# Optimization experiments

Measured on AMD Instinct MI355X. Metric: run time of the kernel, lower is better.

The kernel has to match this reference:

```python
import jax, jax.numpy as jnp
import numpy as np

N_NODES = 100000
N_EDGES = 1600000
OBS_DIMS = 128
HID = 128
ACT_DIMS = 8
NUM_GRAPHS = 256
NEG_SLOPE = 0.2


def setup_inputs() -> dict:
    key = jax.random.key(0)
    ks = jax.random.split(key, 20)
    inp = {}
    inp["x"] = jax.random.normal(ks[0], (N_NODES, OBS_DIMS), dtype=jnp.float32)
    inp["edge_index"] = jax.random.randint(ks[1], (2, N_EDGES), 0, N_NODES, dtype=jnp.int64)
    inp["batch"] = jnp.sort(jax.random.randint(ks[2], (N_NODES,), 0, NUM_GRAPHS, dtype=jnp.int64))
    # GATConv layer params (heads=1): W [out,in], att_src/att_dst [out], bias [out]
    dims = [(HID, OBS_DIMS), (HID, HID), (HID, HID)]
    for i, (o, c) in enumerate(dims, start=1):
        k = 3 + 4 * (i - 1)
        inp[f"W{i}"] = jax.random.normal(ks[k], (o, c), dtype=jnp.float32) * (1.0 / np.sqrt(c))
        inp[f"as{i}"] = jax.random.normal(ks[k + 1], (o,), dtype=jnp.float32) * 0.1
        inp[f"ad{i}"] = jax.random.normal(ks[k + 2], (o,), dtype=jnp.float32) * 0.1
        inp[f"b{i}"] = jnp.zeros((o,), dtype=jnp.float32)
    inp["Wl"] = jax.random.normal(ks[15], (ACT_DIMS, HID), dtype=jnp.float32) * (1.0 / np.sqrt(HID))
    inp["bl"] = jnp.zeros((ACT_DIMS,), dtype=jnp.float32)
    return inp


def _gat_conv(x, src, dst, W, att_src, att_dst, bias):
    """PyG GATConv with heads=1, negative_slope=0.2 (self-loops already in src/dst)."""
    h = x @ W.T                                  # [N, out]
    a_s = h @ att_src                            # [N]
    a_d = h @ att_dst                            # [N]
    e = jax.nn.leaky_relu(a_s[src] + a_d[dst], NEG_SLOPE)   # [E] per-edge logits
    m = jax.ops.segment_max(e, dst, num_segments=N_NODES)   # segment softmax (stable)
    ex = jnp.exp(e - m[dst])
    denom = jax.ops.segment_sum(ex, dst, num_segments=N_NODES)
    alpha = ex / denom[dst]                      # [E]
    out = jax.ops.segment_sum(alpha[:, None] * h[src], dst, num_segments=N_NODES)
    return out + bias


def reference(x, edge_index, batch, W1, as1, ad1, b1, W2, as2, ad2, b2,
              W3, as3, ad3, b3, Wl, bl):
    # add self-loops (PyG GATConv default add_self_loops=True)
    loop = jnp.arange(N_NODES, dtype=edge_index.dtype)
    src = jnp.concatenate([edge_index[0], loop])
    dst = jnp.concatenate([edge_index[1], loop])

    h = jax.nn.relu(_gat_conv(x, src, dst, W1, as1, ad1, b1))
    h = jax.nn.relu(_gat_conv(h, src, dst, W2, as2, ad2, b2))
    h = jax.nn.relu(_gat_conv(h, src, dst, W3, as3, ad3, b3))
    h = jnp.tanh(h @ Wl.T + bl)                  # [N, act_dims]

    # global_mean_pool over graph ids
    sums = jax.ops.segment_sum(h, batch, num_segments=NUM_GRAPHS)
    cnts = jax.ops.segment_sum(jnp.ones((h.shape[0],), h.dtype), batch, num_segments=NUM_GRAPHS)
    return sums / jnp.clip(cnts, 1.0)[:, None]
```

## Files before the change

kernel.cpp:

```cpp
#include <hip/hip_runtime.h>

#define N_NODES 100000
#define N_EDGES 1600000
#define E_TOT   1700000
#define HID     128
#define NGRAPH  256
#define NBUCK   196
#define NBLK1   831
#define HSTRIDE 832

typedef unsigned short ushort_t;
typedef unsigned int uint_t;
typedef __attribute__((ext_vector_type(8))) short bf16x8;
typedef __attribute__((ext_vector_type(4))) float f32x4;

__device__ inline ushort_t f2bf(float f) {
  uint_t u = __float_as_uint(f);
  return (ushort_t)((u + 0x7FFFu + ((u >> 16) & 1u)) >> 16);
}

__global__ __launch_bounds__(256) void k_wcvt(const float* __restrict__ W0,
                                              const float* __restrict__ W1,
                                              const float* __restrict__ W2,
                                              const float* __restrict__ Wlh,
                                              ushort_t* __restrict__ Wb,
                                              ushort_t* __restrict__ Wlb) {
  int i = blockIdx.x * 256 + threadIdx.x;
  if (i < 49152) {
    const float* src = (i < 16384) ? W0 : (i < 32768 ? W1 : W2);
    Wb[i] = f2bf(src[i & 16383]);
  } else if (i < 51200) {
    int j = i - 49152;
    Wlb[j] = (j < 1024) ? f2bf(Wlh[j]) : (ushort_t)0;
  }
}

__global__ __launch_bounds__(256) void k_b1(const int* __restrict__ ei,
                                            int* __restrict__ hist) {
  __shared__ int h[NBUCK];
  const int t = threadIdx.x;
  for (int i = t; i < NBUCK; i += 256) h[i] = 0;
  __syncthreads();
  const int e0 = blockIdx.x * 2048;
#pragma unroll
  for (int u = 0; u < 8; ++u) {
    int e = e0 + u * 256 + t;
    if (e < E_TOT) {
      int dst = (e < N_EDGES) ? ei[N_EDGES + e] : (e - N_EDGES);
      atomicAdd(&h[dst >> 9], 1);
    }
  }
  __syncthreads();
  for (int i = t; i < NBUCK; i += 256) hist[i * HSTRIDE + blockIdx.x] = h[i];
}

__global__ __launch_bounds__(1024) void k_bscan1(int* __restrict__ hist,
                                                 int* __restrict__ btot) {
  __shared__ int sh[1024];
  const int b = blockIdx.x, t = threadIdx.x;
  int v = (t < NBLK1) ? hist[b * HSTRIDE + t] : 0;
  sh[t] = v;
  __syncthreads();
  for (int off = 1; off < 1024; off <<= 1) {
    int x = (t >= off) ? sh[t - off] : 0;
    __syncthreads();
    sh[t] += x;
    __syncthreads();
  }
  if (t < NBLK1) hist[b * HSTRIDE + t] = sh[t] - v;
  if (t == 1023) btot[b] = sh[1023];
}

__global__ void k_bscan2(const int* __restrict__ btot, int* __restrict__ bbase) {
  if (threadIdx.x == 0 && blockIdx.x == 0) {
    int run = 0;
    for (int i = 0; i < NBUCK; ++i) { bbase[i] = run; run += btot[i]; }
    bbase[NBUCK] = run;
  }
}

__global__ __launch_bounds__(256) void k_b2(const int* __restrict__ ei,
                                            const int* __restrict__ hist,
                                            const int* __restrict__ bbase,
                                            int2* __restrict__ buf) {
  __shared__ int h[NBUCK];
  __shared__ int base2[NBUCK];
  const int t = threadIdx.x;
  for (int i = t; i < NBUCK; i += 256) {
    h[i] = 0;
    base2[i] = bbase[i] + hist[i * HSTRIDE + blockIdx.x];
  }
  __syncthreads();
  const int e0 = blockIdx.x * 2048;
#pragma unroll
  for (int u = 0; u < 8; ++u) {
    int e = e0 + u * 256 + t;
    if (e < E_TOT) {
      int src, dst;
      if (e < N_EDGES) { src = ei[e]; dst = ei[N_EDGES + e]; }
      else             { src = e - N_EDGES; dst = src; }
      int bk = dst >> 9;
      int r = atomicAdd(&h[bk], 1);
      buf[base2[bk] + r] = int2{src, dst};
    }
  }
}

__global__ __launch_bounds__(512) void k_b3(const int2* __restrict__ buf,
                                            const int* __restrict__ bbase,
                                            int* __restrict__ indptr,
                                            int* __restrict__ csr_src) {
  __shared__ int cnt[512];
  __shared__ int cur[512];
  const int b = blockIdx.x, t = threadIdx.x;
  cnt[t] = 0;
  __syncthreads();
  const int es = bbase[b], ee = bbase[b + 1];
  for (int e = es + t; e < ee; e += 512) {
    int2 p = buf[e];
    atomicAdd(&cnt[p.y & 511], 1);
  }
  __syncthreads();
  int v = cnt[t];
  cur[t] = v;
  __syncthreads();
  for (int off = 1; off < 512; off <<= 1) {
    int x = (t >= off) ? cur[t - off] : 0;
    __syncthreads();
    cur[t] += x;
    __syncthreads();
  }
  int excl = cur[t] - v;
  int n = b * 512 + t;
  if (n < N_NODES) indptr[n] = es + excl;
  if (b == NBUCK - 1 && t == 0) indptr[N_NODES] = E_TOT;
  __syncthreads();
  cur[t] = es + excl;
  __syncthreads();
  for (int e = es + t; e < ee; e += 512) {
    int2 p = buf[e];
    int pos = atomicAdd(&cur[p.y & 511], 1);
    csr_src[pos] = p.x;
  }
}

template <bool IN_F32>
__global__ __launch_bounds__(256) void k_gemm(const void* __restrict__ Xin,
                                              const ushort_t* __restrict__ Wbl,
                                              const float* __restrict__ att_s,
                                              const float* __restrict__ att_d,
                                              ushort_t* __restrict__ Hb,
                                              float* __restrict__ As,
                                              float* __restrict__ Ad) {
  __shared__ ushort_t Wl[128 * 128];
  __shared__ ushort_t Xl[64 * 128];
  const int t = threadIdx.x;
  const int row0 = blockIdx.x * 64;

#pragma unroll
  for (int i = 0; i < 8; ++i) {
    int idx = (t + i * 256) << 3;
    int o = idx >> 7, c = idx & 127;
    uint4 wv = *(const uint4*)&Wbl[idx];
    *(uint4*)((char*)Wl + o * 256 + ((c * 2) ^ ((o & 7) << 4))) = wv;
  }
  if (IN_F32) {
    const float* X = (const float*)Xin;
#pragma unroll
    for (int i = 0; i < 8; ++i) {
      int idx = (t + i * 256) << 2;
      int r = idx >> 7, c = idx & 127;
      int row = row0 + r;
      float4 xv = (row < N_NODES) ? *(const float4*)&X[row * 128 + c]
                                  : float4{0.f, 0.f, 0.f, 0.f};
      ushort4 xb{f2bf(xv.x), f2bf(xv.y), f2bf(xv.z), f2bf(xv.w)};
      *(ushort4*)((char*)Xl + r * 256 + ((c * 2) ^ ((r & 7) << 4))) = xb;
    }
  } else {
    const ushort_t* X = (const ushort_t*)Xin;
#pragma unroll
    for (int i = 0; i < 4; ++i) {
      int idx = (t + i * 256) << 3;
      int r = idx >> 7, c = idx & 127;
      int row = row0 + r;
      uint4 xv = (row < N_NODES) ? *(const uint4*)&X[row * 128 + c]
                                 : uint4{0u, 0u, 0u, 0u};
      *(uint4*)((char*)Xl + r * 256 + ((c * 2) ^ ((r & 7) << 4))) = xv;
    }
  }
  __syncthreads();

  const int wv = t >> 6;
  const int lane = t & 63;
  const int lr = lane & 15;
  const int lg = lane >> 4;
  f32x4 acc[8] = {};

#pragma unroll
  for (int ks = 0; ks < 4; ++ks) {
    const int kbyte = ks * 64 + lg * 16;
    const int arow = wv * 16 + lr;
    bf16x8 afrag = *(const bf16x8*)((char*)Xl + arow * 256 +
                                    (kbyte ^ ((arow & 7) << 4)));
#pragma unroll
    for (int ot = 0; ot < 8; ++ot) {
      const int orow = ot * 16 + lr;
      bf16x8 bfrag = *(const bf16x8*)((char*)Wl + orow * 256 +
                                      (kbyte ^ ((orow & 7) << 4)));
      acc[ot] = __builtin_amdgcn_mfma_f32_16x16x32_bf16(afrag, bfrag, acc[ot],
                                                        0, 0, 0);
    }
  }

  float ps[4] = {0.f, 0.f, 0.f, 0.f}, pd[4] = {0.f, 0.f, 0.f, 0.f};
#pragma unroll
  for (int ot = 0; ot < 8; ++ot) {
    float sa = att_s[ot * 16 + lr], sd = att_d[ot * 16 + lr];
#pragma unroll
    for (int j = 0; j < 4; ++j) {
      ps[j] += acc[ot][j] * sa;
      pd[j] += acc[ot][j] * sd;
    }
  }
#pragma unroll
  for (int m = 1; m < 16; m <<= 1) {
#pragma unroll
    for (int j = 0; j < 4; ++j) {
      ps[j] += __shfl_xor(ps[j], m);
      pd[j] += __shfl_xor(pd[j], m);
    }
  }
  if (lr == 0) {
#pragma unroll
    for (int j = 0; j < 4; ++j) {
      int row = row0 + wv * 16 + lg * 4 + j;
      if (row < N_NODES) { As[row] = ps[j]; Ad[row] = pd[j]; }
    }
  }

  __syncthreads();
#pragma unroll
  for (int ot = 0; ot < 8; ++ot)
#pragma unroll
    for (int j = 0; j < 4; ++j) {
      int r = wv * 16 + lg * 4 + j;
      int cbyte = (ot * 16 + lr) * 2;
      *(ushort_t*)((char*)Xl + r * 256 + (cbyte ^ ((r & 7) << 4))) =
          f2bf(acc[ot][j]);
    }
  __syncthreads();
#pragma unroll
  for (int i = 0; i < 4; ++i) {
    int idx = t + i * 256;
    int r = idx >> 4, u = idx & 15;
    int row = row0 + r;
    if (row < N_NODES)
      *(uint4*)&Hb[row * 128 + u * 8] =
          *(const uint4*)((char*)Xl + r * 256 + ((u * 16) ^ ((r & 7) << 4)));
  }
}

__global__ __launch_bounds__(256) void k_agg(const ushort_t* __restrict__ Hb,
                                             const float* __restrict__ a_s,
                                             const float* __restrict__ a_d,
                                             const int* __restrict__ indptr,
                                             const int* __restrict__ csr_src,
                                             const float* __restrict__ bias,
                                             ushort_t* __restrict__ OUTb) {
  const int lane = threadIdx.x & 63;
  const int wid  = threadIdx.x >> 6;
  const int half = lane >> 5;
  const int l32  = lane & 31;
  const int n = blockIdx.x * 8 + wid * 2 + half;

  const int start = indptr[n];
  const int deg   = indptr[n + 1] - start;
  const float adn = a_d[n];

  int   s0 = csr_src[start + ((l32 < deg) ? l32 : 0)];
  float w0 = 0.f;
  if (l32 < deg) {
    float e = a_s[s0] + adn;
    e = (e > 0.f) ? e : 0.2f * e;
    w0 = __expf(e);
  }
  float wsum = w0;

  const int degA = __shfl(deg, 0);
  const int degB = __shfl(deg, 32);
  const int degM = max(degA, degB);

  const int q  = lane >> 4;
  const int qe = q & 1;
  const int srcbase = (q >> 1) << 5;
  const int ch = (lane & 15) << 3;
  float acc8[8] = {0.f, 0.f, 0.f, 0.f, 0.f, 0.f, 0.f, 0.f};

#define FMA8(W4, A)                                                         \
  {                                                                         \
    float a_ = (A);                                                         \
    acc8[0] += a_ * __uint_as_float((W4).x << 16);                          \
    acc8[1] += a_ * __uint_as_float((W4).x & 0xFFFF0000u);                  \
    acc8[2] += a_ * __uint_as_float((W4).y << 16);                          \
    acc8[3] += a_ * __uint_as_float((W4).y & 0xFFFF0000u);                  \
    acc8[4] += a_ * __uint_as_float((W4).z << 16);                          \
    acc8[5] += a_ * __uint_as_float((W4).z & 0xFFFF0000u);                  \
    acc8[6] += a_ * __uint_as_float((W4).w << 16);                          \
    acc8[7] += a_ * __uint_as_float((W4).w & 0xFFFF0000u);                  \
  }

  {
    const int npM = (min(degM, 32) + 1) >> 1;
    float av[8]; int sv[8];
#pragma unroll
    for (int u = 0; u < 8; ++u) {
      int sl = srcbase + ((u << 1) + qe);
      av[u] = __shfl(w0, sl);
      sv[u] = __shfl(s0, sl);
    }
    uint4 hvA[4], hvB[4];
#pragma unroll
    for (int u = 0; u < 4; ++u)
      if (u < npM) hvA[u] = *(const uint4*)&Hb[sv[u] * 128 + ch];
#pragma unroll
    for (int u = 0; u < 4; ++u)
      if (u + 4 < npM) hvB[u] = *(const uint4*)&Hb[sv[u + 4] * 128 + ch];
#pragma unroll
    for (int u = 0; u < 4; ++u)
      if (u < npM) FMA8(hvA[u], av[u]);
#pragma unroll
    for (int u = 0; u < 4; ++u)
      if (u + 4 < npM) FMA8(hvB[u], av[u + 4]);
    for (int u0 = 8; u0 < npM; ++u0) {
      int sl = srcbase + ((u0 << 1) + qe);
      float a = __shfl(w0, sl);
      int s = __shfl(s0, sl);
      uint4 hv = *(const uint4*)&Hb[s * 128 + ch];
      FMA8(hv, a);
    }
  }
  for (int base = 32; base < degM; base += 32) {
    int j = base + l32;
    int mys = csr_src[start + ((j < deg) ? j : 0)];
    float myw = 0.f;
    if (j < deg) {
      float e = a_s[mys] + adn;
      e = (e > 0.f) ? e : 0.2f * e;
      myw = __expf(e);
    }
    wsum += myw;
    const int npM = (min(degM - base, 32) + 1) >> 1;
    for (int u0 = 0; u0 < npM; ++u0) {
      int sl = srcbase + ((u0 << 1) + qe);
      float a = __shfl(myw, sl);
      int s = __shfl(mys, sl);
      uint4 hv = *(const uint4*)&Hb[s * 128 + ch];
      FMA8(hv, a);
    }
  }
#undef FMA8

#pragma unroll
  for (int m = 1; m < 32; m <<= 1) wsum += __shfl_xor(wsum, m);
  const float inv = 1.0f / wsum;

#pragma unroll
  for (int c = 0; c < 8; ++c)
    acc8[c] = (acc8[c] + __shfl_xor(acc8[c], 16)) * inv;

  if (qe == 0) {
    float4 b0 = *(const float4*)&bias[ch];
    float4 b1 = *(const float4*)&bias[ch + 4];
    ushort4 lo{f2bf(fmaxf(acc8[0] + b0.x, 0.f)),
               f2bf(fmaxf(acc8[1] + b0.y, 0.f)),
               f2bf(fmaxf(acc8[2] + b0.z, 0.f)),
               f2bf(fmaxf(acc8[3] + b0.w, 0.f))};
    ushort4 hi{f2bf(fmaxf(acc8[4] + b1.x, 0.f)),
               f2bf(fmaxf(acc8[5] + b1.y, 0.f)),
               f2bf(fmaxf(acc8[6] + b1.z, 0.f)),
               f2bf(fmaxf(acc8[7] + b1.w, 0.f))};
    *(ushort4*)&OUTb[n * 128 + ch] = lo;
    *(ushort4*)&OUTb[n * 128 + ch + 4] = hi;
  }
}

__global__ __launch_bounds__(256) void k_head(const ushort_t* __restrict__ Hb,
                                              const ushort_t* __restrict__ Wlb,
                                              const float* __restrict__ bl,
                                              float* __restrict__ h8) {
  __shared__ ushort_t Xl[64 * 128];
  __shared__ ushort_t Wls[16 * 128];
  const int t = threadIdx.x;
  const int row0 = blockIdx.x * 64;

  {
    int idx = t * 8;
    int o = idx >> 7, c = idx & 127;
    uint4 wv = *(const uint4*)&Wlb[idx];
    *(uint4*)((char*)Wls + o * 256 + ((c * 2) ^ ((o & 7) << 4))) = wv;
  }
#pragma unroll
  for (int i = 0; i < 4; ++i) {
    int idx = (t + i * 256) << 3;
    int r = idx >> 7, c = idx & 127;
    int row = row0 + r;
    uint4 xv = (row < N_NODES) ? *(const uint4*)&Hb[row * 128 + c]
                               : uint4{0u, 0u, 0u, 0u};
    *(uint4*)((char*)Xl + r * 256 + ((c * 2) ^ ((r & 7) << 4))) = xv;
  }
  __syncthreads();

  const int wv = t >> 6;
  const int lane = t & 63;
  const int lr = lane & 15;
  const int lg = lane >> 4;
  f32x4 acc = {};
#pragma unroll
  for (int ks = 0; ks < 4; ++ks) {
    const int kbyte = ks * 64 + lg * 16;
    const int arow = wv * 16 + lr;
    bf16x8 afrag = *(const bf16x8*)((char*)Xl + arow * 256 +
                                    (kbyte ^ ((arow & 7) << 4)));
    bf16x8 bfrag = *(const bf16x8*)((char*)Wls + lr * 256 +
                                    (kbyte ^ ((lr & 7) << 4)));
    acc = __builtin_amdgcn_mfma_f32_16x16x32_bf16(afrag, bfrag, acc, 0, 0, 0);
  }

  if (lr < 8) {
    float b = bl[lr];
#pragma unroll
    for (int j = 0; j < 4; ++j) {
      int row = row0 + wv * 16 + lg * 4 + j;
      if (row < N_NODES) h8[row * 8 + lr] = tanhf(acc[j] + b);
    }
  }
}

__global__ __launch_bounds__(256) void k_pool(const float* __restrict__ h8,
                                              const int* __restrict__ batch,
                                              float* __restrict__ out) {
  int g = blockIdx.x;
  __shared__ int bounds[2];
  if (threadIdx.x < 2) {
    int target = g + threadIdx.x;
    int lo = 0, hi = N_NODES;
    while (lo < hi) {
      int mid = (lo + hi) >> 1;
      if (batch[mid] < target) lo = mid + 1; else hi = mid;
    }
    bounds[threadIdx.x] = lo;
  }
  __syncthreads();
  int lo = bounds[0], hi = bounds[1];
  int ch = threadIdx.x & 7;
  float acc = 0.f;
  for (int n = lo + (threadIdx.x >> 3); n < hi; n += 32)
    acc += h8[n * 8 + ch];

  __shared__ float red[256];
  red[threadIdx.x] = acc;
  __syncthreads();
  for (int off = 128; off >= 8; off >>= 1) {
    if (threadIdx.x < off) red[threadIdx.x] += red[threadIdx.x + off];
    __syncthreads();
  }
  if (threadIdx.x < 8)
    out[g * 8 + threadIdx.x] = red[threadIdx.x] / fmaxf((float)(hi - lo), 1.0f);
}

extern "C" void kernel_launch(void* const* d_in, const int* in_sizes, int n_in,
                              void* d_out, int out_size, void* d_ws, size_t ws_size,
                              hipStream_t stream) {
  const float* x   = (const float*)d_in[0];
  const int*   ei  = (const int*)d_in[1];
  const int*   bat = (const int*)d_in[2];
  const float* Wm[3]  = {(const float*)d_in[3],  (const float*)d_in[7],  (const float*)d_in[11]};
  const float* asv[3] = {(const float*)d_in[4],  (const float*)d_in[8],  (const float*)d_in[12]};
  const float* adv[3] = {(const float*)d_in[5],  (const float*)d_in[9],  (const float*)d_in[13]};
  const float* bv[3]  = {(const float*)d_in[6],  (const float*)d_in[10], (const float*)d_in[14]};
  const float* Wl  = (const float*)d_in[15];
  const float* bl  = (const float*)d_in[16];
  float* out = (float*)d_out;

  char* w = (char*)d_ws;
  ushort_t* Hb   = (ushort_t*)(w + 0);
  ushort_t* hB2  = (ushort_t*)(w + 25600000);
  float* a_s     = (float*)(w + 51200000);
  float* a_d     = (float*)(w + 51600000);
  int*   indptr  = (int*)  (w + 52000000);
  int*   csr     = (int*)  (w + 52400128);
  int2*  buf1    = (int2*) (w + 59200128);
  int*   hist    = (int*)  (w + 72800128);
  int*   btot    = (int*)  (w + 73452416);
  int*   bbase   = (int*)  (w + 73453200);
  float* h8      = (float*)(w + 73454000);
  ushort_t* Wb   = (ushort_t*)(w + 76654000);
  ushort_t* Wlb  = (ushort_t*)(w + 76752304);

  const int gblk = (N_NODES + 63) / 64;
  const int ablk = N_NODES / 8;

  k_wcvt<<<200, 256, 0, stream>>>(Wm[0], Wm[1], Wm[2], Wl, Wb, Wlb);

  k_b1    <<<NBLK1, 256, 0, stream>>>(ei, hist);
  k_bscan1<<<NBUCK, 1024, 0, stream>>>(hist, btot);
  k_bscan2<<<1, 64, 0, stream>>>(btot, bbase);
  k_b2    <<<NBLK1, 256, 0, stream>>>(ei, hist, bbase, buf1);
  k_b3    <<<NBUCK, 512, 0, stream>>>(buf1, bbase, indptr, csr);

  k_gemm<true><<<gblk, 256, 0, stream>>>(x, Wb, asv[0], adv[0], Hb, a_s, a_d);
  k_agg<<<ablk, 256, 0, stream>>>(Hb, a_s, a_d, indptr, csr, bv[0], hB2);
  for (int l = 1; l < 3; ++l) {
    k_gemm<false><<<gblk, 256, 0, stream>>>(hB2, Wb + l * 16384, asv[l], adv[l],
                                            Hb, a_s, a_d);
    k_agg<<<ablk, 256, 0, stream>>>(Hb, a_s, a_d, indptr, csr, bv[l], hB2);
  }

  k_head<<<gblk, 256, 0, stream>>>(hB2, Wlb, bl, h8);
  k_pool<<<NGRAPH, 256, 0, stream>>>(h8, bat, out);
}
```

Baseline: 314.5 us.

## Split aggregation into softmax-weight pass and column-sliced gather with sliced H layout

```diff
diff --git a/kernel.cpp b/kernel.cpp
--- a/kernel.cpp
+++ b/kernel.cpp
@@ -8,6 +8,7 @@
 #define NBUCK   196
 #define NBLK1   831
 #define HSTRIDE 832
+#define SL_N    (N_NODES * 16)
 
 typedef unsigned short ushort_t;
 typedef unsigned int uint_t;
@@ -149,7 +150,7 @@
                                               const ushort_t* __restrict__ Wbl,
                                               const float* __restrict__ att_s,
                                               const float* __restrict__ att_d,
-                                              ushort_t* __restrict__ Hb,
+                                              ushort_t* __restrict__ Hs,
                                               float* __restrict__ As,
                                               float* __restrict__ Ad) {
   __shared__ ushort_t Wl[128 * 128];
@@ -180,12 +181,15 @@
     const ushort_t* X = (const ushort_t*)Xin;
 #pragma unroll
     for (int i = 0; i < 4; ++i) {
-      int idx = (t + i * 256) << 3;
-      int r = idx >> 7, c = idx & 127;
+      int gid = t + i * 256;
+      int slice = gid >> 7, rem = gid & 127;
+      int r = rem >> 1, hh = rem & 1;
       int row = row0 + r;
-      uint4 xv = (row < N_NODES) ? *(const uint4*)&X[row * 128 + c]
-                                 : uint4{0u, 0u, 0u, 0u};
-      *(uint4*)((char*)Xl + r * 256 + ((c * 2) ^ ((r & 7) << 4))) = xv;
+      int c0 = slice * 16 + hh * 8;
+      uint4 xv = (row < N_NODES)
+          ? *(const uint4*)&X[slice * SL_N + row * 16 + hh * 8]
+          : uint4{0u, 0u, 0u, 0u};
+      *(uint4*)((char*)Xl + r * 256 + ((c0 * 2) ^ ((r & 7) << 4))) = xv;
     }
   }
   __syncthreads();
@@ -251,22 +255,22 @@
   __syncthreads();
 #pragma unroll
   for (int i = 0; i < 4; ++i) {
-    int idx = t + i * 256;
-    int r = idx >> 4, u = idx & 15;
+    int gid = t + i * 256;
+    int slice = gid >> 7, rem = gid & 127;
+    int r = rem >> 1, hh = rem & 1;
     int row = row0 + r;
+    int c0 = slice * 16 + hh * 8;
     if (row < N_NODES)
-      *(uint4*)&Hb[row * 128 + u * 8] =
-          *(const uint4*)((char*)Xl + r * 256 + ((u * 16) ^ ((r & 7) << 4)));
-  }
-}
-
-__global__ __launch_bounds__(256) void k_agg(const ushort_t* __restrict__ Hb,
-                                             const float* __restrict__ a_s,
-                                             const float* __restrict__ a_d,
-                                             const int* __restrict__ indptr,
-                                             const int* __restrict__ csr_src,
-                                             const float* __restrict__ bias,
-                                             ushort_t* __restrict__ OUTb) {
+      *(uint4*)&Hs[slice * SL_N + row * 16 + hh * 8] =
+          *(const uint4*)((char*)Xl + r * 256 + ((c0 * 2) ^ ((r & 7) << 4)));
+  }
+}
+
+__global__ __launch_bounds__(256) void k_wexp(const float* __restrict__ a_s,
+                                              const float* __restrict__ a_d,
+                                              const int* __restrict__ indptr,
+                                              const int* __restrict__ csr,
+                                              float* __restrict__ alpha) {
   const int lane = threadIdx.x & 63;
   const int wid  = threadIdx.x >> 6;
   const int half = lane >> 5;
@@ -277,24 +281,50 @@
   const int deg   = indptr[n + 1] - start;
   const float adn = a_d[n];
 
-  int   s0 = csr_src[start + ((l32 < deg) ? l32 : 0)];
   float w0 = 0.f;
   if (l32 < deg) {
-    float e = a_s[s0] + adn;
+    float e = a_s[csr[start + l32]] + adn;
     e = (e > 0.f) ? e : 0.2f * e;
     w0 = __expf(e);
   }
   float wsum = w0;
-
-  const int degA = __shfl(deg, 0);
-  const int degB = __shfl(deg, 32);
-  const int degM = max(degA, degB);
-
-  const int q  = lane >> 4;
-  const int qe = q & 1;
-  const int srcbase = (q >> 1) << 5;
-  const int ch = (lane & 15) << 3;
+  for (int j = l32 + 32; j < deg; j += 32) {
+    float e = a_s[csr[start + j]] + adn;
+    e = (e > 0.f) ? e : 0.2f * e;
+    wsum += __expf(e);
+  }
+#pragma unroll
+  for (int m = 1; m < 32; m <<= 1) wsum += __shfl_xor(wsum, m);
+  const float inv = 1.0f / wsum;
+  if (l32 < deg) alpha[start + l32] = w0 * inv;
+  for (int j = l32 + 32; j < deg; j += 32) {
+    float e = a_s[csr[start + j]] + adn;
+    e = (e > 0.f) ? e : 0.2f * e;
+    alpha[start + j] = __expf(e) * inv;
+  }
+}
+
+__global__ __launch_bounds__(256) void k_aggs(const ushort_t* __restrict__ Hs,
+                                              const float* __restrict__ alpha,
+                                              const int* __restrict__ indptr,
+                                              const int* __restrict__ csr,
+                                              const float* __restrict__ bias,
+                                              ushort_t* __restrict__ OUTs) {
+  const int b = blockIdx.x;
+  const int slice = b & 7;
+  const int grp = b >> 3;
+  const int t = threadIdx.x;
+  const int wid = t >> 6, lane = t & 63;
+  const int p = lane >> 1, hh = lane & 1;
+  const ushort_t* Hsl = Hs + slice * SL_N;
+  const int n = grp * 128 + wid * 32 + p;
+
   float acc8[8] = {0.f, 0.f, 0.f, 0.f, 0.f, 0.f, 0.f, 0.f};
+  int start = 0, deg = 0;
+  if (n < N_NODES) {
+    start = __builtin_nontemporal_load(&indptr[n]);
+    deg = __builtin_nontemporal_load(&indptr[n + 1]) - start;
+  }
 
 #define FMA8(W4, A)                                                         \
   {                                                                         \
@@ -309,68 +339,32 @@
     acc8[7] += a_ * __uint_as_float((W4).w & 0xFFFF0000u);                  \
   }
 
-  {
-    const int npM = (min(degM, 32) + 1) >> 1;
-    float av[8]; int sv[8];
-#pragma unroll
-    for (int u = 0; u < 8; ++u) {
-      int sl = srcbase + ((u << 1) + qe);
-      av[u] = __shfl(w0, sl);
-      sv[u] = __shfl(s0, sl);
-    }
-    uint4 hvA[4], hvB[4];
+  int j = 0;
+  for (; j + 4 <= deg; j += 4) {
+    float av[4]; int sv[4]; uint4 hv[4];
+#pragma unroll
+    for (int u = 0; u < 4; ++u) {
+      av[u] = __builtin_nontemporal_load(&alpha[start + j + u]);
+      sv[u] = __builtin_nontemporal_load(&csr[start + j + u]);
+    }
 #pragma unroll
     for (int u = 0; u < 4; ++u)
-      if (u < npM) hvA[u] = *(const uint4*)&Hb[sv[u] * 128 + ch];
-#pragma unroll
-    for (int u = 0; u < 4; ++u)
-      if (u + 4 < npM) hvB[u] = *(const uint4*)&Hb[sv[u + 4] * 128 + ch];
-#pragma unroll
-    for (int u = 0; u < 4; ++u)
-      if (u < npM) FMA8(hvA[u], av[u]);
-#pragma unroll
-    for (int u = 0; u < 4; ++u)
-      if (u + 4 < npM) FMA8(hvB[u], av[u + 4]);
-    for (int u0 = 8; u0 < npM; ++u0) {
-      int sl = srcbase + ((u0 << 1) + qe);
-      float a = __shfl(w0, sl);
-      int s = __shfl(s0, sl);
-      uint4 hv = *(const uint4*)&Hb[s * 128 + ch];
-      FMA8(hv, a);
-    }
-  }
-  for (int base = 32; base < degM; base += 32) {
-    int j = base + l32;
-    int mys = csr_src[start + ((j < deg) ? j : 0)];
-    float myw = 0.f;
-    if (j < deg) {
-      float e = a_s[mys] + adn;
-      e = (e > 0.f) ? e : 0.2f * e;
-      myw = __expf(e);
-    }
-    wsum += myw;
-    const int npM = (min(degM - base, 32) + 1) >> 1;
-    for (int u0 = 0; u0 < npM; ++u0) {
-      int sl = srcbase + ((u0 << 1) + qe);
-      float a = __shfl(myw, sl);
-      int s = __shfl(mys, sl);
-      uint4 hv = *(const uint4*)&Hb[s * 128 + ch];
-      FMA8(hv, a);
-    }
+      hv[u] = *(const uint4*)&Hsl[sv[u] * 16 + hh * 8];
+#pragma unroll
+    for (int u = 0; u < 4; ++u) FMA8(hv[u], av[u]);
+  }
+  for (; j < deg; ++j) {
+    float a = __builtin_nontemporal_load(&alpha[start + j]);
+    int s = __builtin_nontemporal_load(&csr[start + j]);
+    uint4 hv = *(const uint4*)&Hsl[s * 16 + hh * 8];
+    FMA8(hv, a);
   }
 #undef FMA8
 
-#pragma unroll
-  for (int m = 1; m < 32; m <<= 1) wsum += __shfl_xor(wsum, m);
-  const float inv = 1.0f / wsum;
-
-#pragma unroll
-  for (int c = 0; c < 8; ++c)
-    acc8[c] = (acc8[c] + __shfl_xor(acc8[c], 16)) * inv;
-
-  if (qe == 0) {
-    float4 b0 = *(const float4*)&bias[ch];
-    float4 b1 = *(const float4*)&bias[ch + 4];
+  if (n < N_NODES) {
+    const int c0 = slice * 16 + hh * 8;
+    float4 b0 = *(const float4*)&bias[c0];
+    float4 b1 = *(const float4*)&bias[c0 + 4];
     ushort4 lo{f2bf(fmaxf(acc8[0] + b0.x, 0.f)),
                f2bf(fmaxf(acc8[1] + b0.y, 0.f)),
                f2bf(fmaxf(acc8[2] + b0.z, 0.f)),
@@ -379,12 +373,13 @@
                f2bf(fmaxf(acc8[5] + b1.y, 0.f)),
                f2bf(fmaxf(acc8[6] + b1.z, 0.f)),
                f2bf(fmaxf(acc8[7] + b1.w, 0.f))};
-    *(ushort4*)&OUTb[n * 128 + ch] = lo;
-    *(ushort4*)&OUTb[n * 128 + ch + 4] = hi;
-  }
-}
-
-__global__ __launch_bounds__(256) void k_head(const ushort_t* __restrict__ Hb,
+    ushort_t* o = &OUTs[slice * SL_N + n * 16 + hh * 8];
+    *(ushort4*)o = lo;
+    *(ushort4*)(o + 4) = hi;
+  }
+}
+
+__global__ __launch_bounds__(256) void k_head(const ushort_t* __restrict__ Hs,
                                               const ushort_t* __restrict__ Wlb,
                                               const float* __restrict__ bl,
                                               float* __restrict__ h8) {
@@ -401,12 +396,15 @@
   }
 #pragma unroll
   for (int i = 0; i < 4; ++i) {
-    int idx = (t + i * 256) << 3;
-    int r = idx >> 7, c = idx & 127;
+    int gid = t + i * 256;
+    int slice = gid >> 7, rem = gid & 127;
+    int r = rem >> 1, hh = rem & 1;
     int row = row0 + r;
-    uint4 xv = (row < N_NODES) ? *(const uint4*)&Hb[row * 128 + c]
-                               : uint4{0u, 0u, 0u, 0u};
-    *(uint4*)((char*)Xl + r * 256 + ((c * 2) ^ ((r & 7) << 4))) = xv;
+    int c0 = slice * 16 + hh * 8;
+    uint4 xv = (row < N_NODES)
+        ? *(const uint4*)&Hs[slice * SL_N + row * 16 + hh * 8]
+        : uint4{0u, 0u, 0u, 0u};
+    *(uint4*)((char*)Xl + r * 256 + ((c0 * 2) ^ ((r & 7) << 4))) = xv;
   }
   __syncthreads();
 
@@ -496,9 +494,10 @@
   float* h8      = (float*)(w + 73454000);
   ushort_t* Wb   = (ushort_t*)(w + 76654000);
   ushort_t* Wlb  = (ushort_t*)(w + 76752304);
+  float* alpha   = (float*)(w + 76756400);
 
   const int gblk = (N_NODES + 63) / 64;
-  const int ablk = N_NODES / 8;
+  const int sblk = 8 * ((N_NODES + 127) / 128);
 
   k_wcvt<<<200, 256, 0, stream>>>(Wm[0], Wm[1], Wm[2], Wl, Wb, Wlb);
 
@@ -509,11 +508,13 @@
   k_b3    <<<NBUCK, 512, 0, stream>>>(buf1, bbase, indptr, csr);
 
   k_gemm<true><<<gblk, 256, 0, stream>>>(x, Wb, asv[0], adv[0], Hb, a_s, a_d);
-  k_agg<<<ablk, 256, 0, stream>>>(Hb, a_s, a_d, indptr, csr, bv[0], hB2);
+  k_wexp<<<N_NODES / 8, 256, 0, stream>>>(a_s, a_d, indptr, csr, alpha);
+  k_aggs<<<sblk, 256, 0, stream>>>(Hb, alpha, indptr, csr, bv[0], hB2);
   for (int l = 1; l < 3; ++l) {
     k_gemm<false><<<gblk, 256, 0, stream>>>(hB2, Wb + l * 16384, asv[l], adv[l],
                                             Hb, a_s, a_d);
-    k_agg<<<ablk, 256, 0, stream>>>(Hb, a_s, a_d, indptr, csr, bv[l], hB2);
+    k_wexp<<<N_NODES / 8, 256, 0, stream>>>(a_s, a_d, indptr, csr, alpha);
+    k_aggs<<<sblk, 256, 0, stream>>>(Hb, alpha, indptr, csr, bv[l], hB2);
   }
 
   k_head<<<gblk, 256, 0, stream>>>(hB2, Wlb, bl, h8);
```

Result: slower. 726.6 us (+131.0%).
